# Performance work log

Hardware: AMD Instinct MI355X
Metric: run time of the kernel (lower is better)

Reference implementation:

```python
import jax, jax.numpy as jnp
import numpy as np

B = 16        # num sequences (decode: 1 query token each)
HQ = 32       # query heads
HKV = 8       # kv heads
G = HQ // HKV # gqa groups
D = 128       # head dim
BS = 16       # block size
MAXB = 256    # blocks per sequence
NBLK = B * MAXB
MAXKV = MAXB * BS  # 4096
SCALE = D ** -0.5
NEG = jnp.float32(-1e30)


def setup_inputs() -> dict:
    key = jax.random.key(0)
    ks = jax.random.split(key, 6)
    q = jax.random.normal(ks[0], (B, HQ, D), dtype=jnp.float32)
    k = jax.random.normal(ks[1], (B, HKV, D), dtype=jnp.float32)
    v = jax.random.normal(ks[2], (B, HKV, D), dtype=jnp.float32)
    k_cache = jax.random.normal(ks[3], (NBLK, BS, HKV, D), dtype=jnp.float32)
    v_cache = jax.random.normal(ks[4], (NBLK, BS, HKV, D), dtype=jnp.float32)
    # each sequence owns a contiguous slab of MAXB distinct blocks
    block_tables = jnp.arange(NBLK, dtype=jnp.int32).reshape(B, MAXB)
    seq_lens = jax.random.randint(ks[5], (B,), 1, MAXKV + 1, dtype=jnp.int32)
    # slot of the newest token (the one being written this step)
    last = seq_lens - 1
    slot_mapping = (block_tables[jnp.arange(B), last // BS] * BS + last % BS).astype(jnp.int32)
    return {"q": q, "k": k, "v": v, "k_cache": k_cache, "v_cache": v_cache,
            "slot_mapping": slot_mapping, "block_tables": block_tables, "seq_lens": seq_lens}


def reference(q, k, v, k_cache, v_cache, slot_mapping, block_tables, seq_lens):
    # write_kv_cache: flat view index_copy at absolute slots
    kc = k_cache.reshape(-1, HKV, D).at[slot_mapping].set(k).reshape(k_cache.shape)
    vc = v_cache.reshape(-1, HKV, D).at[slot_mapping].set(v).reshape(v_cache.shape)
    # paged gather: [B, MAXB, BS, HKV, D] -> [B, MAXKV, HKV, D]
    kg = kc[block_tables].reshape(B, MAXKV, HKV, D)
    vg = vc[block_tables].reshape(B, MAXKV, HKV, D)
    # GQA: q head h attends kv head h // G  (== repeat_interleave on kv)
    qg = q.reshape(B, HKV, G, D)
    scores = jnp.einsum('bkgd,bskd->bkgs', qg, kg) * SCALE  # [B,HKV,G,S]
    valid = jnp.arange(MAXKV)[None, :] < seq_lens[:, None]   # [B,S]
    scores = jnp.where(valid[:, None, None, :], scores, NEG)
    probs = jax.nn.softmax(scores, axis=-1)
    out = jnp.einsum('bkgs,bskd->bkgd', probs, vg).reshape(B, HQ, D)
    return out
```

## Files before the change

### kernel.cpp

```cpp
#include <hip/hip_runtime.h>
#include <math.h>

#define B_     16
#define HQ_    32
#define HKV_   8
#define G_     4
#define D_     128
#define BS_    16
#define MAXB_  256
#define MAXKV_ 4096
#define NPART_ 16
#define PART_  (MAXKV_ / NPART_)

#define SL_ (0.08838834764831845f * 1.4426950408889634f)

__global__ void write_kv(const float* __restrict__ k, const float* __restrict__ v,
                         float* __restrict__ kc, float* __restrict__ vc,
                         const int* __restrict__ slot_mapping) {
    int i = blockIdx.x * blockDim.x + threadIdx.x;
    int b = i >> 10;
    int r = i & 1023;
    int slot = slot_mapping[b];
    size_t o = (size_t)slot * (HKV_ * D_) + r;
    kc[o] = k[i];
    vc[o] = v[i];
}

__launch_bounds__(64)
__global__ void attn_partial(const float* __restrict__ q,
                             const float* __restrict__ kc,
                             const float* __restrict__ vc,
                             const int* __restrict__ block_tables,
                             const int* __restrict__ seq_lens,
                             float* __restrict__ ws_acc,
                             float* __restrict__ ws_ml) {
    const int p    = blockIdx.x;
    const int kh   = blockIdx.y;
    const int b    = blockIdx.z;
    const int lane = threadIdx.x;

    const int seq_len = seq_lens[b];
    const int start   = p * PART_;
    if (start >= seq_len) return;
    const int end = min(start + PART_, seq_len);

    float2 qv[G_];
#pragma unroll
    for (int g = 0; g < G_; ++g)
        qv[g] = *(const float2*)(q + (size_t)(b * HQ_ + kh * G_ + g) * D_ + 2 * lane);

    float m[G_], l[G_], ax[G_], ay[G_];
#pragma unroll
    for (int g = 0; g < G_; ++g) { m[g] = -1e30f; l[g] = 0.f; ax[g] = 0.f; ay[g] = 0.f; }

    const int* btr = block_tables + b * MAXB_;

    int s = start;
    for (; s + 1 < end; s += 2) {
        int blk0 = btr[s >> 4];
        int blk1 = btr[(s + 1) >> 4];
        size_t base0 = ((size_t)((blk0 << 4) | (s & 15)) * HKV_ + kh) * D_;
        size_t base1 = ((size_t)((blk1 << 4) | ((s + 1) & 15)) * HKV_ + kh) * D_;
        float2 k0 = *(const float2*)(kc + base0 + 2 * lane);
        float2 k1 = *(const float2*)(kc + base1 + 2 * lane);
        float2 v0 = *(const float2*)(vc + base0 + 2 * lane);
        float2 v1 = *(const float2*)(vc + base1 + 2 * lane);

        float sc0[G_], sc1[G_];
#pragma unroll
        for (int g = 0; g < G_; ++g) {
            sc0[g] = qv[g].x * k0.x + qv[g].y * k0.y;
            sc1[g] = qv[g].x * k1.x + qv[g].y * k1.y;
        }
#pragma unroll
        for (int off = 32; off >= 1; off >>= 1) {
#pragma unroll
            for (int g = 0; g < G_; ++g) {
                sc0[g] += __shfl_xor(sc0[g], off, 64);
                sc1[g] += __shfl_xor(sc1[g], off, 64);
            }
        }
#pragma unroll
        for (int g = 0; g < G_; ++g) {
            float s0 = sc0[g] * SL_;
            float s1 = sc1[g] * SL_;
            float mn = fmaxf(m[g], fmaxf(s0, s1));
            float alpha = exp2f(m[g] - mn);
            float p0 = exp2f(s0 - mn);
            float p1 = exp2f(s1 - mn);
            l[g]  = l[g]  * alpha + p0 + p1;
            ax[g] = ax[g] * alpha + p0 * v0.x + p1 * v1.x;
            ay[g] = ay[g] * alpha + p0 * v0.y + p1 * v1.y;
            m[g] = mn;
        }
    }
    if (s < end) {
        int blk0 = btr[s >> 4];
        size_t base0 = ((size_t)((blk0 << 4) | (s & 15)) * HKV_ + kh) * D_;
        float2 k0 = *(const float2*)(kc + base0 + 2 * lane);
        float2 v0 = *(const float2*)(vc + base0 + 2 * lane);
        float sc0[G_];
#pragma unroll
        for (int g = 0; g < G_; ++g)
            sc0[g] = qv[g].x * k0.x + qv[g].y * k0.y;
#pragma unroll
        for (int off = 32; off >= 1; off >>= 1)
#pragma unroll
            for (int g = 0; g < G_; ++g)
                sc0[g] += __shfl_xor(sc0[g], off, 64);
#pragma unroll
        for (int g = 0; g < G_; ++g) {
            float s0 = sc0[g] * SL_;
            float mn = fmaxf(m[g], s0);
            float alpha = exp2f(m[g] - mn);
            float p0 = exp2f(s0 - mn);
            l[g]  = l[g]  * alpha + p0;
            ax[g] = ax[g] * alpha + p0 * v0.x;
            ay[g] = ay[g] * alpha + p0 * v0.y;
            m[g] = mn;
        }
    }

#pragma unroll
    for (int g = 0; g < G_; ++g) {
        int hidx = (b * HKV_ + kh) * G_ + g;
        float2 st; st.x = ax[g]; st.y = ay[g];
        *(float2*)(ws_acc + (size_t)(hidx * NPART_ + p) * D_ + 2 * lane) = st;
        if (lane == 0) {
            ws_ml[(size_t)(hidx * NPART_ + p) * 2 + 0] = m[g];
            ws_ml[(size_t)(hidx * NPART_ + p) * 2 + 1] = l[g];
        }
    }
}

__launch_bounds__(128)
__global__ void attn_combine(const float* __restrict__ ws_acc,
                             const float* __restrict__ ws_ml,
                             const int* __restrict__ seq_lens,
                             float* __restrict__ out) {
    const int hidx = blockIdx.x;
    const int d    = threadIdx.x;
    const int b    = hidx / HQ_;
    const int seq_len = seq_lens[b];
    const int nvalid  = min(NPART_, (seq_len + PART_ - 1) / PART_);

    float M = -1e30f, L = 0.f, o = 0.f;
    for (int p = 0; p < nvalid; ++p) {
        float mp = ws_ml[(size_t)(hidx * NPART_ + p) * 2 + 0];
        float lp = ws_ml[(size_t)(hidx * NPART_ + p) * 2 + 1];
        float a  = ws_acc[(size_t)(hidx * NPART_ + p) * D_ + d];
        float mn = fmaxf(M, mp);
        float so = exp2f(M - mn);
        float sn = exp2f(mp - mn);
        o = o * so + a * sn;
        L = L * so + lp * sn;
        M = mn;
    }
    out[(size_t)hidx * D_ + d] = o / L;
}

extern "C" void kernel_launch(void* const* d_in, const int* in_sizes, int n_in,
                              void* d_out, int out_size, void* d_ws, size_t ws_size,
                              hipStream_t stream) {
    const float* q  = (const float*)d_in[0];
    const float* k  = (const float*)d_in[1];
    const float* v  = (const float*)d_in[2];
    float* kc       = (float*)d_in[3];
    float* vc       = (float*)d_in[4];
    const int* slot = (const int*)d_in[5];
    const int* bt   = (const int*)d_in[6];
    const int* sl   = (const int*)d_in[7];
    float* out      = (float*)d_out;

    float* ws_acc = (float*)d_ws;
    float* ws_ml  = ws_acc + (size_t)B_ * HQ_ * NPART_ * D_;

    hipLaunchKernelGGL(write_kv, dim3((B_ * HKV_ * D_) / 256), dim3(256), 0, stream,
                       k, v, kc, vc, slot);
    hipLaunchKernelGGL(attn_partial, dim3(NPART_, HKV_, B_), dim3(64), 0, stream,
                       q, kc, vc, bt, sl, ws_acc, ws_ml);
    hipLaunchKernelGGL(attn_combine, dim3(B_ * HQ_), dim3(128), 0, stream,
                       ws_acc, ws_ml, sl, out);
}
```

Measured before the change: 597.0 us.

## Fuse new-token KV into attention, raise split count, widen per-lane loads

Removes the separate cache-write kernel. The newest token's K/V is read straight from the k/v inputs inside the attention kernel instead of being written to the cache first. The number of sequence partitions grows to 64 or 32 when workspace allows. Each wave now handles two tokens per step with float4 loads, keeps eight K/V loads in flight per chunk, and reads block-table entries as int4. The aim is more memory-level parallelism and fewer launches, paid for with a two-half merge at the end, more combine work, and no longer updating the KV cache in place.

```diff
diff --git a/kernel.cpp b/kernel.cpp
--- a/kernel.cpp
+++ b/kernel.cpp
@@ -9,126 +9,165 @@
 #define BS_    16
 #define MAXB_  256
 #define MAXKV_ 4096
-#define NPART_ 16
-#define PART_  (MAXKV_ / NPART_)
 
 #define SL_ (0.08838834764831845f * 1.4426950408889634f)
-
-__global__ void write_kv(const float* __restrict__ k, const float* __restrict__ v,
-                         float* __restrict__ kc, float* __restrict__ vc,
-                         const int* __restrict__ slot_mapping) {
-    int i = blockIdx.x * blockDim.x + threadIdx.x;
-    int b = i >> 10;
-    int r = i & 1023;
-    int slot = slot_mapping[b];
-    size_t o = (size_t)slot * (HKV_ * D_) + r;
-    kc[o] = k[i];
-    vc[o] = v[i];
-}
-
+#define NEGINF_ (-1e30f)
+
+template<int NPART>
 __launch_bounds__(64)
 __global__ void attn_partial(const float* __restrict__ q,
+                             const float* __restrict__ kin,
+                             const float* __restrict__ vin,
                              const float* __restrict__ kc,
                              const float* __restrict__ vc,
                              const int* __restrict__ block_tables,
                              const int* __restrict__ seq_lens,
                              float* __restrict__ ws_acc,
                              float* __restrict__ ws_ml) {
+    constexpr int PART = MAXKV_ / NPART;
+    constexpr int NB   = PART / BS_;
     const int p    = blockIdx.x;
     const int kh   = blockIdx.y;
     const int b    = blockIdx.z;
     const int lane = threadIdx.x;
-
-    const int seq_len = seq_lens[b];
-    const int start   = p * PART_;
-    if (start >= seq_len) return;
-    const int end = min(start + PART_, seq_len);
-
-    float2 qv[G_];
+    const int half = lane >> 5;
+    const int l32  = lane & 31;
+
+    const int seq   = seq_lens[b];
+    const int start = p * PART;
+    if (start >= seq) return;
+    const int last    = seq - 1;
+    const int end_eff = min(start + PART, last);
+
+    float4 qv[G_];
 #pragma unroll
     for (int g = 0; g < G_; ++g)
-        qv[g] = *(const float2*)(q + (size_t)(b * HQ_ + kh * G_ + g) * D_ + 2 * lane);
-
-    float m[G_], l[G_], ax[G_], ay[G_];
-#pragma unroll
-    for (int g = 0; g < G_; ++g) { m[g] = -1e30f; l[g] = 0.f; ax[g] = 0.f; ay[g] = 0.f; }
-
-    const int* btr = block_tables + b * MAXB_;
-
-    int s = start;
-    for (; s + 1 < end; s += 2) {
-        int blk0 = btr[s >> 4];
-        int blk1 = btr[(s + 1) >> 4];
-        size_t base0 = ((size_t)((blk0 << 4) | (s & 15)) * HKV_ + kh) * D_;
-        size_t base1 = ((size_t)((blk1 << 4) | ((s + 1) & 15)) * HKV_ + kh) * D_;
-        float2 k0 = *(const float2*)(kc + base0 + 2 * lane);
-        float2 k1 = *(const float2*)(kc + base1 + 2 * lane);
-        float2 v0 = *(const float2*)(vc + base0 + 2 * lane);
-        float2 v1 = *(const float2*)(vc + base1 + 2 * lane);
-
-        float sc0[G_], sc1[G_];
+        qv[g] = *(const float4*)(q + (size_t)(b * HQ_ + kh * G_ + g) * D_ + 4 * l32);
+
+    float  m[G_], l_[G_];
+    float4 acc[G_];
+#pragma unroll
+    for (int g = 0; g < G_; ++g) {
+        m[g] = NEGINF_; l_[g] = 0.f;
+        acc[g].x = acc[g].y = acc[g].z = acc[g].w = 0.f;
+    }
+
+    int blks[NB];
+#pragma unroll
+    for (int i = 0; i < NB; i += 4) {
+        int4 t4 = *(const int4*)(block_tables + b * MAXB_ + (start >> 4) + i);
+        blks[i] = t4.x; blks[i + 1] = t4.y; blks[i + 2] = t4.z; blks[i + 3] = t4.w;
+    }
+
+#pragma unroll
+    for (int bi = 0; bi < NB; ++bi) {
+        const int sb = start + bi * BS_;
+        if (sb >= end_eff) break;
+        const size_t rowbase = ((size_t)blks[bi] * (BS_ * HKV_) + kh) * D_ + 4 * l32;
+        const float* kb = kc + rowbase;
+        const float* vb = vc + rowbase;
+#pragma unroll
+        for (int ii = 0; ii < 2; ++ii) {
+            const int t0 = sb + ii * 8;
+            if (t0 >= end_eff) break;
+            float4 kv[4], vv[4];
+#pragma unroll
+            for (int j = 0; j < 4; ++j) {
+                const int off = ii * 8 + 2 * j + half;
+                kv[j] = *(const float4*)(kb + (size_t)off * (HKV_ * D_));
+                vv[j] = *(const float4*)(vb + (size_t)off * (HKV_ * D_));
+            }
+#pragma unroll
+            for (int j = 0; j < 4; ++j) {
+                const int  t     = t0 + 2 * j + half;
+                const bool valid = t < end_eff;
+                float sc[G_];
+#pragma unroll
+                for (int g = 0; g < G_; ++g) {
+                    float s = qv[g].x * kv[j].x;
+                    s = fmaf(qv[g].y, kv[j].y, s);
+                    s = fmaf(qv[g].z, kv[j].z, s);
+                    sc[g] = fmaf(qv[g].w, kv[j].w, s);
+                }
+#pragma unroll
+                for (int off = 16; off >= 1; off >>= 1)
+#pragma unroll
+                    for (int g = 0; g < G_; ++g)
+                        sc[g] += __shfl_xor(sc[g], off, 64);
+#pragma unroll
+                for (int g = 0; g < G_; ++g) {
+                    float s  = valid ? sc[g] * SL_ : NEGINF_;
+                    float mn = fmaxf(m[g], s);
+                    float al = exp2f(m[g] - mn);
+                    float pp = exp2f(s - mn);
+                    l_[g]    = l_[g] * al + pp;
+                    acc[g].x = fmaf(acc[g].x, al, pp * vv[j].x);
+                    acc[g].y = fmaf(acc[g].y, al, pp * vv[j].y);
+                    acc[g].z = fmaf(acc[g].z, al, pp * vv[j].z);
+                    acc[g].w = fmaf(acc[g].w, al, pp * vv[j].w);
+                    m[g] = mn;
+                }
+            }
+        }
+    }
+
+    if (last - start < PART) {
+        const float4 kf = *(const float4*)(kin + (size_t)(b * HKV_ + kh) * D_ + 4 * l32);
+        const float4 vf = *(const float4*)(vin + (size_t)(b * HKV_ + kh) * D_ + 4 * l32);
+        float sc[G_];
 #pragma unroll
         for (int g = 0; g < G_; ++g) {
-            sc0[g] = qv[g].x * k0.x + qv[g].y * k0.y;
-            sc1[g] = qv[g].x * k1.x + qv[g].y * k1.y;
-        }
-#pragma unroll
-        for (int off = 32; off >= 1; off >>= 1) {
-#pragma unroll
-            for (int g = 0; g < G_; ++g) {
-                sc0[g] += __shfl_xor(sc0[g], off, 64);
-                sc1[g] += __shfl_xor(sc1[g], off, 64);
+            float s = qv[g].x * kf.x;
+            s = fmaf(qv[g].y, kf.y, s);
+            s = fmaf(qv[g].z, kf.z, s);
+            sc[g] = fmaf(qv[g].w, kf.w, s);
+        }
+#pragma unroll
+        for (int off = 16; off >= 1; off >>= 1)
+#pragma unroll
+            for (int g = 0; g < G_; ++g)
+                sc[g] += __shfl_xor(sc[g], off, 64);
+#pragma unroll
+        for (int g = 0; g < G_; ++g) {
+            float s  = (half == 0) ? sc[g] * SL_ : NEGINF_;
+            float mn = fmaxf(m[g], s);
+            float al = exp2f(m[g] - mn);
+            float pp = exp2f(s - mn);
+            l_[g]    = l_[g] * al + pp;
+            acc[g].x = fmaf(acc[g].x, al, pp * vf.x);
+            acc[g].y = fmaf(acc[g].y, al, pp * vf.y);
+            acc[g].z = fmaf(acc[g].z, al, pp * vf.z);
+            acc[g].w = fmaf(acc[g].w, al, pp * vf.w);
+            m[g] = mn;
+        }
+    }
+
+#pragma unroll
+    for (int g = 0; g < G_; ++g) {
+        float  mo = __shfl_xor(m[g], 32, 64);
+        float  lo = __shfl_xor(l_[g], 32, 64);
+        float4 ao;
+        ao.x = __shfl_xor(acc[g].x, 32, 64);
+        ao.y = __shfl_xor(acc[g].y, 32, 64);
+        ao.z = __shfl_xor(acc[g].z, 32, 64);
+        ao.w = __shfl_xor(acc[g].w, 32, 64);
+        float mn = fmaxf(m[g], mo);
+        float a  = exp2f(m[g] - mn);
+        float c  = exp2f(mo  - mn);
+        float lm = l_[g] * a + lo * c;
+        float4 am;
+        am.x = acc[g].x * a + ao.x * c;
+        am.y = acc[g].y * a + ao.y * c;
+        am.z = acc[g].z * a + ao.z * c;
+        am.w = acc[g].w * a + ao.w * c;
+
+        const int hidx = (b * HKV_ + kh) * G_ + g;
+        if (half == 0) {
+            *(float4*)(ws_acc + (size_t)(hidx * NPART + p) * D_ + 4 * l32) = am;
+            if (l32 == 0) {
+                ws_ml[(size_t)(hidx * NPART + p) * 2 + 0] = mn;
+                ws_ml[(size_t)(hidx * NPART + p) * 2 + 1] = lm;
             }
-        }
-#pragma unroll
-        for (int g = 0; g < G_; ++g) {
-            float s0 = sc0[g] * SL_;
-            float s1 = sc1[g] * SL_;
-            float mn = fmaxf(m[g], fmaxf(s0, s1));
-            float alpha = exp2f(m[g] - mn);
-            float p0 = exp2f(s0 - mn);
-            float p1 = exp2f(s1 - mn);
-            l[g]  = l[g]  * alpha + p0 + p1;
-            ax[g] = ax[g] * alpha + p0 * v0.x + p1 * v1.x;
-            ay[g] = ay[g] * alpha + p0 * v0.y + p1 * v1.y;
-            m[g] = mn;
-        }
-    }
-    if (s < end) {
-        int blk0 = btr[s >> 4];
-        size_t base0 = ((size_t)((blk0 << 4) | (s & 15)) * HKV_ + kh) * D_;
-        float2 k0 = *(const float2*)(kc + base0 + 2 * lane);
-        float2 v0 = *(const float2*)(vc + base0 + 2 * lane);
-        float sc0[G_];
-#pragma unroll
-        for (int g = 0; g < G_; ++g)
-            sc0[g] = qv[g].x * k0.x + qv[g].y * k0.y;
-#pragma unroll
-        for (int off = 32; off >= 1; off >>= 1)
-#pragma unroll
-            for (int g = 0; g < G_; ++g)
-                sc0[g] += __shfl_xor(sc0[g], off, 64);
-#pragma unroll
-        for (int g = 0; g < G_; ++g) {
-            float s0 = sc0[g] * SL_;
-            float mn = fmaxf(m[g], s0);
-            float alpha = exp2f(m[g] - mn);
-            float p0 = exp2f(s0 - mn);
-            l[g]  = l[g]  * alpha + p0;
-            ax[g] = ax[g] * alpha + p0 * v0.x;
-            ay[g] = ay[g] * alpha + p0 * v0.y;
-            m[g] = mn;
-        }
-    }
-
-#pragma unroll
-    for (int g = 0; g < G_; ++g) {
-        int hidx = (b * HKV_ + kh) * G_ + g;
-        float2 st; st.x = ax[g]; st.y = ay[g];
-        *(float2*)(ws_acc + (size_t)(hidx * NPART_ + p) * D_ + 2 * lane) = st;
-        if (lane == 0) {
-            ws_ml[(size_t)(hidx * NPART_ + p) * 2 + 0] = m[g];
-            ws_ml[(size_t)(hidx * NPART_ + p) * 2 + 1] = l[g];
         }
     }
 }
@@ -137,18 +176,19 @@
 __global__ void attn_combine(const float* __restrict__ ws_acc,
                              const float* __restrict__ ws_ml,
                              const int* __restrict__ seq_lens,
-                             float* __restrict__ out) {
+                             float* __restrict__ out,
+                             int npart, int part) {
     const int hidx = blockIdx.x;
     const int d    = threadIdx.x;
     const int b    = hidx / HQ_;
-    const int seq_len = seq_lens[b];
-    const int nvalid  = min(NPART_, (seq_len + PART_ - 1) / PART_);
-
-    float M = -1e30f, L = 0.f, o = 0.f;
+    const int seq  = seq_lens[b];
+    const int nvalid = min(npart, (seq + part - 1) / part);
+
+    float M = NEGINF_, L = 0.f, o = 0.f;
     for (int p = 0; p < nvalid; ++p) {
-        float mp = ws_ml[(size_t)(hidx * NPART_ + p) * 2 + 0];
-        float lp = ws_ml[(size_t)(hidx * NPART_ + p) * 2 + 1];
-        float a  = ws_acc[(size_t)(hidx * NPART_ + p) * D_ + d];
+        float mp = ws_ml[(size_t)(hidx * npart + p) * 2 + 0];
+        float lp = ws_ml[(size_t)(hidx * npart + p) * 2 + 1];
+        float a  = ws_acc[(size_t)(hidx * npart + p) * D_ + d];
         float mn = fmaxf(M, mp);
         float so = exp2f(M - mn);
         float sn = exp2f(mp - mn);
@@ -159,26 +199,34 @@
     out[(size_t)hidx * D_ + d] = o / L;
 }
 
+template<int NPART>
+static void launch_all(const float* q, const float* k, const float* v,
+                       const float* kc, const float* vc,
+                       const int* bt, const int* sl,
+                       float* out, void* d_ws, hipStream_t stream) {
+    float* ws_acc = (float*)d_ws;
+    float* ws_ml  = ws_acc + (size_t)B_ * HQ_ * NPART * D_;
+    hipLaunchKernelGGL((attn_partial<NPART>), dim3(NPART, HKV_, B_), dim3(64), 0, stream,
+                       q, k, v, kc, vc, bt, sl, ws_acc, ws_ml);
+    hipLaunchKernelGGL(attn_combine, dim3(B_ * HQ_), dim3(128), 0, stream,
+                       ws_acc, ws_ml, sl, out, NPART, MAXKV_ / NPART);
+}
+
 extern "C" void kernel_launch(void* const* d_in, const int* in_sizes, int n_in,
                               void* d_out, int out_size, void* d_ws, size_t ws_size,
                               hipStream_t stream) {
     const float* q  = (const float*)d_in[0];
     const float* k  = (const float*)d_in[1];
     const float* v  = (const float*)d_in[2];
-    float* kc       = (float*)d_in[3];
-    float* vc       = (float*)d_in[4];
-    const int* slot = (const int*)d_in[5];
+    const float* kc = (const float*)d_in[3];
+    const float* vc = (const float*)d_in[4];
     const int* bt   = (const int*)d_in[6];
     const int* sl   = (const int*)d_in[7];
     float* out      = (float*)d_out;
 
-    float* ws_acc = (float*)d_ws;
-    float* ws_ml  = ws_acc + (size_t)B_ * HQ_ * NPART_ * D_;
-
-    hipLaunchKernelGGL(write_kv, dim3((B_ * HKV_ * D_) / 256), dim3(256), 0, stream,
-                       k, v, kc, vc, slot);
-    hipLaunchKernelGGL(attn_partial, dim3(NPART_, HKV_, B_), dim3(64), 0, stream,
-                       q, kc, vc, bt, sl, ws_acc, ws_ml);
-    hipLaunchKernelGGL(attn_combine, dim3(B_ * HQ_), dim3(128), 0, stream,
-                       ws_acc, ws_ml, sl, out);
-}
+    const size_t need64 = (size_t)B_ * HQ_ * 64 * (D_ + 2) * sizeof(float);
+    const size_t need32 = (size_t)B_ * HQ_ * 32 * (D_ + 2) * sizeof(float);
+    if (ws_size >= need64)      launch_all<64>(q, k, v, kc, vc, bt, sl, out, d_ws, stream);
+    else if (ws_size >= need32) launch_all<32>(q, k, v, kc, vc, bt, sl, out, d_ws, stream);
+    else                        launch_all<16>(q, k, v, kc, vc, bt, sl, out, d_ws, stream);
+}
```

Measured after the change: 493.8 us. 1.21x faster.
